# Kernel optimization log

Measured on AMD Instinct MI355X. Metric: run time of the kernel, lower is better.

Reference implementation:

```python
import jax, jax.numpy as jnp
import numpy as np

K = 3  # involution kernel size


def dwconv3x3(x, w, b):
    # x: [B,C,H,W], w: [C,1,3,3] (depthwise, groups=C), b: [C]
    y = jax.lax.conv_general_dilated(
        x, w, window_strides=(1, 1), padding='SAME',
        dimension_numbers=('NCHW', 'OIHW', 'NCHW'),
        feature_group_count=x.shape[1])
    return y + b[None, :, None, None]


def conv1x1(x, w, b):
    # x: [B,C,H,W], w: [O,C], b: [O]
    return jnp.einsum('oc,bchw->bohw', w, x) + b[None, :, None, None]


def extract_patches(x):
    # x: [B,C,H,W] -> [B,C,K*K,H,W], zero-padded 'same' 3x3 neighborhoods
    B, C, H, W = x.shape
    p = (K - 1) // 2
    xp = jnp.pad(x, ((0, 0), (0, 0), (p, p), (p, p)))
    return jnp.stack([xp[:, :, i:i + H, j:j + W]
                      for i in range(K) for j in range(K)], axis=2)


def involution(x, w_red, b_red, w_span, b_span):
    # dynamic per-pixel kernels: [B, K*K, H, W]
    kern = conv1x1(jax.nn.relu(conv1x1(x, w_red, b_red)), w_span, b_span)
    patches = extract_patches(x)                 # [B,C,KK,H,W]
    return jnp.einsum('bkhw,bckhw->bchw', kern, patches)


def setup_inputs() -> dict:
    key = jax.random.key(0)
    ks = jax.random.split(key, 10)
    dim, red = 256, 64  # reduction ratio 4
    B, H, W = 8, 64, 64
    s = 0.05
    return {
        'x': jax.random.normal(ks[0], (B, dim, H, W), jnp.float32),
        'w_in': jax.random.normal(ks[1], (dim, 1, 3, 3), jnp.float32) * s,
        'b_in': jax.random.normal(ks[2], (dim,), jnp.float32) * s,
        'w_red': jax.random.normal(ks[3], (red, dim), jnp.float32) * s,
        'b_red': jax.random.normal(ks[4], (red,), jnp.float32) * s,
        'w_span': jax.random.normal(ks[5], (K * K, red), jnp.float32) * s,
        'b_span': jax.random.normal(ks[6], (K * K,), jnp.float32) * s,
        'w_out': jax.random.normal(ks[7], (dim, 1, 3, 3), jnp.float32) * s,
        'b_out': jax.random.normal(ks[8], (dim,), jnp.float32) * s,
    }


def reference(x, w_in, b_in, w_red, b_red, w_span, b_span, w_out, b_out):
    x = dwconv3x3(x, w_in, b_in)
    x = involution(x, w_red, b_red, w_span, b_span)
    x = dwconv3x3(x, w_out, b_out)
    return x
```

## Files before the change

kernel.cpp:

```cpp
#include <hip/hip_runtime.h>

#define BB 8
#define CC 256
#define HH 64
#define WW 64
#define RED 64
#define HW 4096
#define XS 68
#define LS 68

__global__ __launch_bounds__(256) void transpose_wred(const float* __restrict__ w_red,
                                                      float* __restrict__ wt) {
    int idx = blockIdx.x * 256 + threadIdx.x;
    int o = idx >> 8, c = idx & 255;
    wt[c * RED + o] = w_red[idx];
}

__global__ __launch_bounds__(512) void dw_kern(const float* __restrict__ x,
                                               const float* __restrict__ w_in,
                                               const float* __restrict__ b_in,
                                               const float* __restrict__ wt,
                                               const float* __restrict__ b_red,
                                               const float* __restrict__ w_span,
                                               const float* __restrict__ b_span,
                                               float* __restrict__ kern) {
    __shared__ float xs[2][64 * XS];
    __shared__ float part[8 * 9 * 64];
    const int t  = threadIdx.x;
    const int bx = blockIdx.x;
    const int h  = ((bx & 7) << 3) | (bx >> 3);
    const int b  = blockIdx.y;
    const int px = t & 63;
    const int og = t >> 6;
    const int o0 = __builtin_amdgcn_readfirstlane(og << 3);
    const int q  = t & 15;
    const int w0 = q << 2;
    const int cr = t >> 4;

    float acc[8];
    #pragma unroll
    for (int i = 0; i < 8; i++) acc[i] = 0.f;

    auto phaseA = [&](int c0, int buf) {
        #pragma unroll
        for (int s = 0; s < 2; s++) {
            const int cl = s * 32 + cr;
            const int cc = c0 + cl;
            const float* xp = x + ((size_t)(b * CC + cc)) * HW;
            const float* wp = w_in + cc * 9;
            const float bb = b_in[cc];
            float4 a4 = make_float4(bb, bb, bb, bb);
            #pragma unroll
            for (int ky = 0; ky < 3; ky++) {
                int hh = h + ky - 1;
                if (hh < 0 || hh >= HH) continue;
                const float* row = xp + hh * WW + w0;
                float4 v = *(const float4*)row;
                float lf = (w0 > 0)      ? row[-1] : 0.f;
                float rt = (w0 + 4 < WW) ? row[4]  : 0.f;
                float k0 = wp[ky * 3 + 0], k1 = wp[ky * 3 + 1], k2 = wp[ky * 3 + 2];
                a4.x = fmaf(k0, lf,  a4.x); a4.y = fmaf(k0, v.x, a4.y);
                a4.z = fmaf(k0, v.y, a4.z); a4.w = fmaf(k0, v.z, a4.w);
                a4.x = fmaf(k1, v.x, a4.x); a4.y = fmaf(k1, v.y, a4.y);
                a4.z = fmaf(k1, v.z, a4.z); a4.w = fmaf(k1, v.w, a4.w);
                a4.x = fmaf(k2, v.y, a4.x); a4.y = fmaf(k2, v.z, a4.y);
                a4.z = fmaf(k2, v.w, a4.z); a4.w = fmaf(k2, rt,  a4.w);
            }
            *(float4*)&xs[buf][cl * XS + w0] = a4;
        }
    };

    phaseA(0, 0);
    __syncthreads();
    for (int k = 0; k < 4; k++) {
        if (k < 3) phaseA((k + 1) << 6, (k + 1) & 1);
        const float* wrow = wt + (k << 6) * RED + o0;
        const float* xb = &xs[k & 1][0];
        #pragma unroll 8
        for (int c = 0; c < 64; c++) {
            float xv = xb[c * XS + px];
            #pragma unroll
            for (int i = 0; i < 8; i++)
                acc[i] = fmaf(wrow[c * RED + i], xv, acc[i]);
        }
        __syncthreads();
    }

    float kk[9];
    #pragma unroll
    for (int j = 0; j < 9; j++) kk[j] = 0.f;
    #pragma unroll
    for (int i = 0; i < 8; i++) {
        float r = fmaxf(acc[i] + b_red[o0 + i], 0.f);
        #pragma unroll
        for (int j = 0; j < 9; j++) kk[j] = fmaf(w_span[j * RED + o0 + i], r, kk[j]);
    }
    #pragma unroll
    for (int j = 0; j < 9; j++) part[(og * 9 + j) * 64 + px] = kk[j];
    __syncthreads();
    if (og == 0) {
        float* kp = kern + (size_t)b * 9 * HW + h * WW + px;
        #pragma unroll
        for (int j = 0; j < 9; j++) {
            float s = b_span[j];
            #pragma unroll
            for (int g = 0; g < 8; g++) s += part[(g * 9 + j) * 64 + px];
            kp[j * HW] = s;
        }
    }
}

__global__ __launch_bounds__(256) void invol_dw(const float* __restrict__ x,
                                                const float* __restrict__ w_in,
                                                const float* __restrict__ b_in,
                                                const float* __restrict__ kern,
                                                const float* __restrict__ w_out,
                                                const float* __restrict__ b_out,
                                                float* __restrict__ out) {
    __shared__ float xs[HH * LS];
    __shared__ float x1s[HH * LS];
    const int t  = threadIdx.x;
    const int q  = t & 15;
    const int w0 = q << 2;
    const int r  = t >> 4;
    const int c = blockIdx.x, b = blockIdx.y;
    const float* xp = x + ((size_t)(b * CC + c)) * HW;

    #pragma unroll
    for (int i = 0; i < 4; i++) {
        int h = r + (i << 4);
        *(float4*)&xs[h * LS + w0] = *(const float4*)(xp + h * WW + w0);
    }
    __syncthreads();

    {
        const float* wp = w_in + c * 9;
        const float bb = b_in[c];
        #pragma unroll
        for (int i = 0; i < 4; i++) {
            int h = r + (i << 4);
            float4 acc = make_float4(bb, bb, bb, bb);
            #pragma unroll
            for (int ky = 0; ky < 3; ky++) {
                int hh = h + ky - 1;
                if (hh < 0 || hh >= HH) continue;
                const float* row = &xs[hh * LS + w0];
                float4 v = *(const float4*)row;
                float lf = (w0 > 0)      ? row[-1] : 0.f;
                float rt = (w0 + 4 < WW) ? row[4]  : 0.f;
                float k0 = wp[ky * 3 + 0], k1 = wp[ky * 3 + 1], k2 = wp[ky * 3 + 2];
                acc.x = fmaf(k0, lf,  acc.x); acc.y = fmaf(k0, v.x, acc.y);
                acc.z = fmaf(k0, v.y, acc.z); acc.w = fmaf(k0, v.z, acc.w);
                acc.x = fmaf(k1, v.x, acc.x); acc.y = fmaf(k1, v.y, acc.y);
                acc.z = fmaf(k1, v.z, acc.z); acc.w = fmaf(k1, v.w, acc.w);
                acc.x = fmaf(k2, v.y, acc.x); acc.y = fmaf(k2, v.z, acc.y);
                acc.z = fmaf(k2, v.w, acc.z); acc.w = fmaf(k2, rt,  acc.w);
            }
            *(float4*)&x1s[h * LS + w0] = acc;
        }
    }
    __syncthreads();

    const float* kp = kern + (size_t)b * 9 * HW;
    #pragma unroll
    for (int i = 0; i < 4; i++) {
        int h  = r + (i << 4);
        int hw = h * WW + w0;
        float4 acc = make_float4(0.f, 0.f, 0.f, 0.f);
        #pragma unroll
        for (int ky = 0; ky < 3; ky++) {
            int hh = h + ky - 1;
            if (hh < 0 || hh >= HH) continue;
            const float* row = &x1s[hh * LS + w0];
            float4 v = *(const float4*)row;
            float lf = (w0 > 0)      ? row[-1] : 0.f;
            float rt = (w0 + 4 < WW) ? row[4]  : 0.f;
            float4 k0 = *(const float4*)(kp + (ky * 3 + 0) * HW + hw);
            float4 k1 = *(const float4*)(kp + (ky * 3 + 1) * HW + hw);
            float4 k2 = *(const float4*)(kp + (ky * 3 + 2) * HW + hw);
            acc.x = fmaf(k0.x, lf,  acc.x); acc.y = fmaf(k0.y, v.x, acc.y);
            acc.z = fmaf(k0.z, v.y, acc.z); acc.w = fmaf(k0.w, v.z, acc.w);
            acc.x = fmaf(k1.x, v.x, acc.x); acc.y = fmaf(k1.y, v.y, acc.y);
            acc.z = fmaf(k1.z, v.z, acc.z); acc.w = fmaf(k1.w, v.w, acc.w);
            acc.x = fmaf(k2.x, v.y, acc.x); acc.y = fmaf(k2.y, v.z, acc.y);
            acc.z = fmaf(k2.z, v.w, acc.z); acc.w = fmaf(k2.w, rt,  acc.w);
        }
        *(float4*)&xs[h * LS + w0] = acc;
    }
    __syncthreads();

    const float* wp = w_out + c * 9;
    const float bb = b_out[c];
    float* op = out + ((size_t)(b * CC + c)) * HW;
    #pragma unroll
    for (int i = 0; i < 4; i++) {
        int h = r + (i << 4);
        float4 acc = make_float4(bb, bb, bb, bb);
        #pragma unroll
        for (int ky = 0; ky < 3; ky++) {
            int hh = h + ky - 1;
            if (hh < 0 || hh >= HH) continue;
            const float* row = &xs[hh * LS + w0];
            float4 v = *(const float4*)row;
            float lf = (w0 > 0)      ? row[-1] : 0.f;
            float rt = (w0 + 4 < WW) ? row[4]  : 0.f;
            float k0 = wp[ky * 3 + 0], k1 = wp[ky * 3 + 1], k2 = wp[ky * 3 + 2];
            acc.x = fmaf(k0, lf,  acc.x); acc.y = fmaf(k0, v.x, acc.y);
            acc.z = fmaf(k0, v.y, acc.z); acc.w = fmaf(k0, v.z, acc.w);
            acc.x = fmaf(k1, v.x, acc.x); acc.y = fmaf(k1, v.y, acc.y);
            acc.z = fmaf(k1, v.z, acc.z); acc.w = fmaf(k1, v.w, acc.w);
            acc.x = fmaf(k2, v.y, acc.x); acc.y = fmaf(k2, v.z, acc.y);
            acc.z = fmaf(k2, v.w, acc.z); acc.w = fmaf(k2, rt,  acc.w);
        }
        *(float4*)(op + h * WW + w0) = acc;
    }
}

extern "C" void kernel_launch(void* const* d_in, const int* in_sizes, int n_in,
                              void* d_out, int out_size, void* d_ws, size_t ws_size,
                              hipStream_t stream) {
    const float* x      = (const float*)d_in[0];
    const float* w_in   = (const float*)d_in[1];
    const float* b_in   = (const float*)d_in[2];
    const float* w_red  = (const float*)d_in[3];
    const float* b_red  = (const float*)d_in[4];
    const float* w_span = (const float*)d_in[5];
    const float* b_span = (const float*)d_in[6];
    const float* w_out  = (const float*)d_in[7];
    const float* b_out  = (const float*)d_in[8];
    float* out = (float*)d_out;

    float* ws   = (float*)d_ws;
    float* kern = ws;
    float* wt   = kern + (size_t)BB * 9 * HW;

    transpose_wred<<<64, 256, 0, stream>>>(w_red, wt);
    dw_kern<<<dim3(HH, BB), 512, 0, stream>>>(x, w_in, b_in, wt, b_red,
                                              w_span, b_span, kern);
    invol_dw<<<dim3(CC, BB), 256, 0, stream>>>(x, w_in, b_in, kern,
                                               w_out, b_out, out);
}
```

Before: 154.7 us.

## Stage reduction weights in LDS and prefetch input rows into registers

The first kernel now stages each 64-channel slice of the transposed reduction weights into a double-buffered LDS region, where it is read as float4 instead of as scalar global loads. The x-buffer becomes a single buffer: the next chunk's input rows are loaded into registers before the 1x1 accumulation and turned into depthwise outputs after it. The partial-sum scratch is aliased onto the same LDS space, and launch bounds ask for four blocks per CU. This trades an extra barrier per chunk and more registers for fewer global weight loads and load latency hidden behind compute.

```diff
diff --git a/kernel.cpp b/kernel.cpp
--- a/kernel.cpp
+++ b/kernel.cpp
@@ -16,16 +16,19 @@
     wt[c * RED + o] = w_red[idx];
 }
 
-__global__ __launch_bounds__(512) void dw_kern(const float* __restrict__ x,
-                                               const float* __restrict__ w_in,
-                                               const float* __restrict__ b_in,
-                                               const float* __restrict__ wt,
-                                               const float* __restrict__ b_red,
-                                               const float* __restrict__ w_span,
-                                               const float* __restrict__ b_span,
-                                               float* __restrict__ kern) {
-    __shared__ float xs[2][64 * XS];
-    __shared__ float part[8 * 9 * 64];
+__global__ __launch_bounds__(512, 4) void dw_kern(const float* __restrict__ x,
+                                                  const float* __restrict__ w_in,
+                                                  const float* __restrict__ b_in,
+                                                  const float* __restrict__ wt,
+                                                  const float* __restrict__ b_red,
+                                                  const float* __restrict__ w_span,
+                                                  const float* __restrict__ b_span,
+                                                  float* __restrict__ kern) {
+    __shared__ float smem[4352 + 2 * 4096];
+    float* xs   = smem;
+    float* wbuf = smem + 4352;
+    float* part = smem;
+
     const int t  = threadIdx.x;
     const int bx = blockIdx.x;
     const int h  = ((bx & 7) << 3) | (bx >> 3);
@@ -37,27 +40,46 @@
     const int w0 = q << 2;
     const int cr = t >> 4;
 
-    float acc[8];
-    #pragma unroll
-    for (int i = 0; i < 8; i++) acc[i] = 0.f;
-
-    auto phaseA = [&](int c0, int buf) {
+    float4 pv[2][3]; float plf[2][3], prt[2][3];
+    float4 wv0, wv1;
+
+    auto loadX = [&](int c0) {
+        #pragma unroll
+        for (int s = 0; s < 2; s++) {
+            const int cc = c0 + s * 32 + cr;
+            const float* xp = x + ((size_t)(b * CC + cc)) * HW;
+            #pragma unroll
+            for (int ky = 0; ky < 3; ky++) {
+                int hh = h + ky - 1;
+                if (hh < 0 || hh >= HH) {
+                    pv[s][ky] = make_float4(0.f, 0.f, 0.f, 0.f);
+                    plf[s][ky] = 0.f; prt[s][ky] = 0.f;
+                    continue;
+                }
+                const float* row = xp + hh * WW + w0;
+                pv[s][ky]  = *(const float4*)row;
+                plf[s][ky] = (w0 > 0)      ? row[-1] : 0.f;
+                prt[s][ky] = (w0 + 4 < WW) ? row[4]  : 0.f;
+            }
+        }
+    };
+    auto loadW = [&](int c0) {
+        const float* wp = wt + c0 * RED + t * 8;
+        wv0 = *(const float4*)wp;
+        wv1 = *(const float4*)(wp + 4);
+    };
+    auto computeX = [&](int c0) {
         #pragma unroll
         for (int s = 0; s < 2; s++) {
             const int cl = s * 32 + cr;
             const int cc = c0 + cl;
-            const float* xp = x + ((size_t)(b * CC + cc)) * HW;
             const float* wp = w_in + cc * 9;
             const float bb = b_in[cc];
             float4 a4 = make_float4(bb, bb, bb, bb);
             #pragma unroll
             for (int ky = 0; ky < 3; ky++) {
-                int hh = h + ky - 1;
-                if (hh < 0 || hh >= HH) continue;
-                const float* row = xp + hh * WW + w0;
-                float4 v = *(const float4*)row;
-                float lf = (w0 > 0)      ? row[-1] : 0.f;
-                float rt = (w0 + 4 < WW) ? row[4]  : 0.f;
+                float4 v = pv[s][ky];
+                float lf = plf[s][ky], rt = prt[s][ky];
                 float k0 = wp[ky * 3 + 0], k1 = wp[ky * 3 + 1], k2 = wp[ky * 3 + 2];
                 a4.x = fmaf(k0, lf,  a4.x); a4.y = fmaf(k0, v.x, a4.y);
                 a4.z = fmaf(k0, v.y, a4.z); a4.w = fmaf(k0, v.z, a4.w);
@@ -66,24 +88,46 @@
                 a4.x = fmaf(k2, v.y, a4.x); a4.y = fmaf(k2, v.z, a4.y);
                 a4.z = fmaf(k2, v.w, a4.z); a4.w = fmaf(k2, rt,  a4.w);
             }
-            *(float4*)&xs[buf][cl * XS + w0] = a4;
-        }
-    };
-
-    phaseA(0, 0);
-    __syncthreads();
+            *(float4*)&xs[cl * XS + w0] = a4;
+        }
+    };
+    auto storeW = [&](int buf) {
+        float* wb = wbuf + buf * 4096 + t * 8;
+        *(float4*)wb = wv0;
+        *(float4*)(wb + 4) = wv1;
+    };
+
+    float acc[8];
+    #pragma unroll
+    for (int i = 0; i < 8; i++) acc[i] = 0.f;
+
+    loadX(0); loadW(0);
+    computeX(0); storeW(0);
+    __syncthreads();
+
     for (int k = 0; k < 4; k++) {
-        if (k < 3) phaseA((k + 1) << 6, (k + 1) & 1);
-        const float* wrow = wt + (k << 6) * RED + o0;
-        const float* xb = &xs[k & 1][0];
+        if (k < 3) { loadX((k + 1) << 6); loadW((k + 1) << 6); }
+        const float* wb = wbuf + (k & 1) * 4096 + o0;
         #pragma unroll 8
         for (int c = 0; c < 64; c++) {
-            float xv = xb[c * XS + px];
-            #pragma unroll
-            for (int i = 0; i < 8; i++)
-                acc[i] = fmaf(wrow[c * RED + i], xv, acc[i]);
+            float xv = xs[c * XS + px];
+            float4 wa = *(const float4*)(wb + c * 64);
+            float4 wc = *(const float4*)(wb + c * 64 + 4);
+            acc[0] = fmaf(wa.x, xv, acc[0]);
+            acc[1] = fmaf(wa.y, xv, acc[1]);
+            acc[2] = fmaf(wa.z, xv, acc[2]);
+            acc[3] = fmaf(wa.w, xv, acc[3]);
+            acc[4] = fmaf(wc.x, xv, acc[4]);
+            acc[5] = fmaf(wc.y, xv, acc[5]);
+            acc[6] = fmaf(wc.z, xv, acc[6]);
+            acc[7] = fmaf(wc.w, xv, acc[7]);
         }
         __syncthreads();
+        if (k < 3) {
+            computeX((k + 1) << 6);
+            storeW((k + 1) & 1);
+            __syncthreads();
+        }
     }
 
     float kk[9];
```

Result: no change. 155.8 us (+0.7%).
